# Performance work log

Hardware: AMD Instinct MI355X
Metric: run time of the kernel (lower is better)

Reference implementation:

```python
import jax, jax.numpy as jnp
import numpy as np

FIELD_DIMS = 100000
FACTORS = 16
BATCH = 1024


def setup_inputs() -> dict:
    key = jax.random.key(0)
    k1, k2 = jax.random.split(key)
    # multi-hot indicator rows (values in {0,1}); row>0 selects active embedding rows
    x0 = jax.random.randint(k1, (BATCH, FIELD_DIMS), 0, 2, dtype=jnp.int32)
    # embedding table (truncated_normal init in the original; plain normal scaled is fine for a numeric reference)
    W = jax.random.normal(k2, (FIELD_DIMS, FACTORS), dtype=jnp.float32) * 0.05
    return {"x0": x0, "W": W}


def reference(x0, W):
    # Original per-row math: let E = W[row > 0] (active embedding rows)
    #   out = 0.5 * ( sum_{i,j} e_i . e_j  -  sum_i ||e_i||^2 )
    # sum_{i,j} e_i . e_j == || sum_i e_i ||^2, so with multi-hot mask m:
    #   s  = m @ W                     -> [B, k]
    #   q  = m @ rowwise_sumsq(W)      -> [B]
    #   out = 0.5 * (||s||^2 - q)      -> [B]
    m = (x0 > 0).astype(W.dtype)                    # [B, F]
    s = m @ W                                        # [B, k]
    q = m @ jnp.sum(W * W, axis=-1)                  # [B]
    return 0.5 * (jnp.sum(s * s, axis=-1) - q)
```

## Files before the change

kernel.cpp:

```cpp
#include <hip/hip_runtime.h>

#define FIELDS  100000
#define FACTORS 16
#define BATCH   1024
#define BT      8
#define NCHUNK  8
#define FPC     (FIELDS / NCHUNK)
#define BLOCK   256
#define TF      256
#define NFULL   (FPC / TF)
#define TAILPG  ((FPC - NFULL * TF) / 4)
#define NBUF    3

typedef __attribute__((address_space(1))) const void gvoid;
typedef __attribute__((address_space(3))) void lvoid;

__global__ __launch_bounds__(BLOCK, 4) void fm_partial(
    const int* __restrict__ x0, const float* __restrict__ W,
    float* __restrict__ ws)
{
    __shared__ __align__(16) int xbuf[NBUF][BT][TF];
    __shared__ float red[4][BT][17];

    const int t     = threadIdx.x;
    const int bid   = blockIdx.x;
    const int rg    = bid >> 3;
    const int chunk = bid & (NCHUNK - 1);
    const int b0    = rg * BT;
    const int fbeg  = chunk * FPC;

    const int qr   = t & 3;
    const int pg   = t >> 2;
    const int lane = t & 63;
    const int wv   = t >> 6;

    float acc[BT][4], qac[BT];
#pragma unroll
    for (int r = 0; r < BT; ++r) {
        qac[r] = 0.f;
#pragma unroll
        for (int j = 0; j < 4; ++j) acc[r][j] = 0.f;
    }

    const char* x0b = (const char*)x0;
    const char* Wb  = (const char*)W;

    const int r0 = 2 * wv, r1 = r0 + 1;
    const unsigned sb0 = ((unsigned)(b0 + r0) * FIELDS + (unsigned)fbeg) * 4u
                       + (unsigned)lane * 16u;
    const unsigned sb1 = sb0 + FIELDS * 4u;
    char* const l0 = (char*)&xbuf[0][r0][0] + lane * 16;
    char* const l1 = (char*)&xbuf[0][r1][0] + lane * 16;

#define STAGE(buf, tile) do {                                               \
        __builtin_amdgcn_global_load_lds(                                   \
            (gvoid*)(x0b + (sb0 + (unsigned)(tile) * (TF * 4u))),           \
            (lvoid*)(l0 + (buf) * (BT * TF * 4)), 16, 0, 0);                \
        __builtin_amdgcn_global_load_lds(                                   \
            (gvoid*)(x0b + (sb1 + (unsigned)(tile) * (TF * 4u))),           \
            (lvoid*)(l1 + (buf) * (BT * TF * 4)), 16, 0, 0);                \
    } while (0)

#define FMTILE(BUFEXPR)                                                     \
    do {                                                                    \
        const float s0 = fmaf(w0.x, w0.x, fmaf(w0.y, w0.y, fmaf(w0.z, w0.z, w0.w * w0.w))); \
        const float s1 = fmaf(w1.x, w1.x, fmaf(w1.y, w1.y, fmaf(w1.z, w1.z, w1.w * w1.w))); \
        const float s2 = fmaf(w2.x, w2.x, fmaf(w2.y, w2.y, fmaf(w2.z, w2.z, w2.w * w2.w))); \
        const float s3 = fmaf(w3.x, w3.x, fmaf(w3.y, w3.y, fmaf(w3.z, w3.z, w3.w * w3.w))); \
        _Pragma("unroll")                                                   \
        for (int r = 0; r < BT; ++r) {                                      \
            const int4 xv = BUFEXPR;                                        \
            const float m0 = (float)xv.x, m1 = (float)xv.y;                 \
            const float m2 = (float)xv.z, m3 = (float)xv.w;                 \
            qac[r]    = fmaf(m0, s0,   fmaf(m1, s1,   fmaf(m2, s2,   fmaf(m3, s3,   qac[r])))); \
            acc[r][0] = fmaf(m0, w0.x, fmaf(m1, w1.x, fmaf(m2, w2.x, fmaf(m3, w3.x, acc[r][0])))); \
            acc[r][1] = fmaf(m0, w0.y, fmaf(m1, w1.y, fmaf(m2, w2.y, fmaf(m3, w3.y, acc[r][1])))); \
            acc[r][2] = fmaf(m0, w0.z, fmaf(m1, w1.z, fmaf(m2, w2.z, fmaf(m3, w3.z, acc[r][2])))); \
            acc[r][3] = fmaf(m0, w0.w, fmaf(m1, w1.w, fmaf(m2, w2.w, fmaf(m3, w3.w, acc[r][3])))); \
        }                                                                   \
    } while (0)

    STAGE(0, 0);
    STAGE(1, 1);

    const unsigned wq = (unsigned)qr * 16u;

    for (int tl = 0; tl < NFULL; ++tl) {
        const unsigned fB = (unsigned)(fbeg + tl * TF + pg * 4) * 64u + wq;
        const float4 w0 = *(const float4*)(Wb + fB);
        const float4 w1 = *(const float4*)(Wb + fB + 64u);
        const float4 w2 = *(const float4*)(Wb + fB + 128u);
        const float4 w3 = *(const float4*)(Wb + fB + 192u);

        if      (tl == 0)         asm volatile("s_waitcnt vmcnt(6)"  ::: "memory");
        else if (tl < NFULL - 1)  asm volatile("s_waitcnt vmcnt(10)" ::: "memory");
        else                      asm volatile("s_waitcnt vmcnt(8)"  ::: "memory");
        __builtin_amdgcn_s_barrier();
        __builtin_amdgcn_sched_barrier(0);

        if (tl + 2 < NFULL) STAGE((tl + 2) % NBUF, tl + 2);

        const int buf = tl % NBUF;
        FMTILE((*(const int4*)&xbuf[buf][r][pg * 4]));
        __builtin_amdgcn_sched_barrier(0);
    }

    {
        const bool valid = (pg < TAILPG);
        const int  pgc   = valid ? pg : (TAILPG - 1);
        const unsigned fb = (unsigned)(fbeg + NFULL * TF + pgc * 4);
        const unsigned wB = fb * 64u + wq;
        float4 w0 = *(const float4*)(Wb + wB);
        float4 w1 = *(const float4*)(Wb + wB + 64u);
        float4 w2 = *(const float4*)(Wb + wB + 128u);
        float4 w3 = *(const float4*)(Wb + wB + 192u);
        if (!valid) {
            w0.x=w0.y=w0.z=w0.w=0.f; w1.x=w1.y=w1.z=w1.w=0.f;
            w2.x=w2.y=w2.z=w2.w=0.f; w3.x=w3.y=w3.z=w3.w=0.f;
        }
        FMTILE((*(const int4*)(x0b + ((unsigned)(b0 + r) * FIELDS + fb) * 4u)));
    }

#pragma unroll
    for (int r = 0; r < BT; ++r) {
#pragma unroll
        for (int off = 4; off < 64; off <<= 1) {
            acc[r][0] += __shfl_xor(acc[r][0], off);
            acc[r][1] += __shfl_xor(acc[r][1], off);
            acc[r][2] += __shfl_xor(acc[r][2], off);
            acc[r][3] += __shfl_xor(acc[r][3], off);
        }
#pragma unroll
        for (int off = 1; off < 64; off <<= 1)
            qac[r] += __shfl_xor(qac[r], off);
    }

    if (lane < 4) {
#pragma unroll
        for (int r = 0; r < BT; ++r) {
#pragma unroll
            for (int j = 0; j < 4; ++j)
                red[wv][r][lane * 4 + j] = acc[r][j];
            if (lane == 0) red[wv][r][16] = qac[r];
        }
    }
    __syncthreads();
    if (t < BT * 17) {
        const int r = t / 17;
        const int j = t % 17;
        const float v = red[0][r][j] + red[1][r][j] + red[2][r][j] + red[3][r][j];
        ws[((size_t)(b0 + r) * NCHUNK + chunk) * 17 + j] = v;
    }
#undef STAGE
#undef FMTILE
}

__global__ __launch_bounds__(BLOCK) void fm_final(
    const float* __restrict__ ws, float* __restrict__ out)
{
    const int b = blockIdx.x * BLOCK + threadIdx.x;
    if (b < BATCH) {
        const float* pbase = ws + (size_t)b * NCHUNK * 17;
        float s[17];
#pragma unroll
        for (int j = 0; j < 17; ++j) s[j] = 0.f;
#pragma unroll
        for (int c = 0; c < NCHUNK; ++c)
#pragma unroll
            for (int j = 0; j < 17; ++j) s[j] += pbase[c * 17 + j];
        float ss = 0.f;
#pragma unroll
        for (int k = 0; k < FACTORS; ++k) ss += s[k] * s[k];
        out[b] = 0.5f * (ss - s[16]);
    }
}

extern "C" void kernel_launch(void* const* d_in, const int* in_sizes, int n_in,
                              void* d_out, int out_size, void* d_ws, size_t ws_size,
                              hipStream_t stream)
{
    const int*   x0 = (const int*)d_in[0];
    const float* W  = (const float*)d_in[1];
    float* out = (float*)d_out;
    float* ws  = (float*)d_ws;

    fm_partial<<<dim3((BATCH / BT) * NCHUNK), dim3(BLOCK), 0, stream>>>(x0, W, ws);
    fm_final<<<dim3((BATCH + BLOCK - 1) / BLOCK), dim3(BLOCK), 0, stream>>>(ws, out);
}
```

Measured before the change: 119.2 us.

## Double tile width to 512 fields with double-buffered LDS staging

Each pipeline step now covers 512 fields instead of 256. Each wave issues four async global-to-LDS loads per step, and each thread loads eight W float4s to cover both halves of the tile. The triple buffer that staged two tiles ahead becomes a double buffer that stages one tile ahead, with a single fixed vmcnt wait. The aim is to halve the barrier and loop overhead and give each wait more bytes in flight, at the cost of a shallower prefetch, more LDS and higher register pressure.

```diff
diff --git a/kernel.cpp b/kernel.cpp
--- a/kernel.cpp
+++ b/kernel.cpp
@@ -7,10 +7,10 @@
 #define NCHUNK  8
 #define FPC     (FIELDS / NCHUNK)
 #define BLOCK   256
-#define TF      256
-#define NFULL   (FPC / TF)
-#define TAILPG  ((FPC - NFULL * TF) / 4)
-#define NBUF    3
+#define TF      512
+#define NTF     (FPC / TF)
+#define TAILPG  ((FPC - NTF * TF) / 4)
+#define NBUF    2
 
 typedef __attribute__((address_space(1))) const void gvoid;
 typedef __attribute__((address_space(3))) void lvoid;
@@ -53,72 +53,80 @@
     char* const l1 = (char*)&xbuf[0][r1][0] + lane * 16;
 
 #define STAGE(buf, tile) do {                                               \
-        __builtin_amdgcn_global_load_lds(                                   \
-            (gvoid*)(x0b + (sb0 + (unsigned)(tile) * (TF * 4u))),           \
+        const unsigned _so = (unsigned)(tile) * (TF * 4u);                  \
+        __builtin_amdgcn_global_load_lds((gvoid*)(x0b + (sb0 + _so)),       \
             (lvoid*)(l0 + (buf) * (BT * TF * 4)), 16, 0, 0);                \
-        __builtin_amdgcn_global_load_lds(                                   \
-            (gvoid*)(x0b + (sb1 + (unsigned)(tile) * (TF * 4u))),           \
+        __builtin_amdgcn_global_load_lds((gvoid*)(x0b + (sb0 + _so + 1024u)),\
+            (lvoid*)(l0 + (buf) * (BT * TF * 4) + 1024), 16, 0, 0);         \
+        __builtin_amdgcn_global_load_lds((gvoid*)(x0b + (sb1 + _so)),       \
             (lvoid*)(l1 + (buf) * (BT * TF * 4)), 16, 0, 0);                \
+        __builtin_amdgcn_global_load_lds((gvoid*)(x0b + (sb1 + _so + 1024u)),\
+            (lvoid*)(l1 + (buf) * (BT * TF * 4) + 1024), 16, 0, 0);         \
     } while (0)
 
-#define FMTILE(BUFEXPR)                                                     \
+#define FMTILE(p0, p1, p2, p3, BUFEXPR)                                     \
     do {                                                                    \
-        const float s0 = fmaf(w0.x, w0.x, fmaf(w0.y, w0.y, fmaf(w0.z, w0.z, w0.w * w0.w))); \
-        const float s1 = fmaf(w1.x, w1.x, fmaf(w1.y, w1.y, fmaf(w1.z, w1.z, w1.w * w1.w))); \
-        const float s2 = fmaf(w2.x, w2.x, fmaf(w2.y, w2.y, fmaf(w2.z, w2.z, w2.w * w2.w))); \
-        const float s3 = fmaf(w3.x, w3.x, fmaf(w3.y, w3.y, fmaf(w3.z, w3.z, w3.w * w3.w))); \
+        const float s0 = fmaf(p0.x, p0.x, fmaf(p0.y, p0.y, fmaf(p0.z, p0.z, p0.w * p0.w))); \
+        const float s1 = fmaf(p1.x, p1.x, fmaf(p1.y, p1.y, fmaf(p1.z, p1.z, p1.w * p1.w))); \
+        const float s2 = fmaf(p2.x, p2.x, fmaf(p2.y, p2.y, fmaf(p2.z, p2.z, p2.w * p2.w))); \
+        const float s3 = fmaf(p3.x, p3.x, fmaf(p3.y, p3.y, fmaf(p3.z, p3.z, p3.w * p3.w))); \
         _Pragma("unroll")                                                   \
         for (int r = 0; r < BT; ++r) {                                      \
             const int4 xv = BUFEXPR;                                        \
             const float m0 = (float)xv.x, m1 = (float)xv.y;                 \
             const float m2 = (float)xv.z, m3 = (float)xv.w;                 \
             qac[r]    = fmaf(m0, s0,   fmaf(m1, s1,   fmaf(m2, s2,   fmaf(m3, s3,   qac[r])))); \
-            acc[r][0] = fmaf(m0, w0.x, fmaf(m1, w1.x, fmaf(m2, w2.x, fmaf(m3, w3.x, acc[r][0])))); \
-            acc[r][1] = fmaf(m0, w0.y, fmaf(m1, w1.y, fmaf(m2, w2.y, fmaf(m3, w3.y, acc[r][1])))); \
-            acc[r][2] = fmaf(m0, w0.z, fmaf(m1, w1.z, fmaf(m2, w2.z, fmaf(m3, w3.z, acc[r][2])))); \
-            acc[r][3] = fmaf(m0, w0.w, fmaf(m1, w1.w, fmaf(m2, w2.w, fmaf(m3, w3.w, acc[r][3])))); \
+            acc[r][0] = fmaf(m0, p0.x, fmaf(m1, p1.x, fmaf(m2, p2.x, fmaf(m3, p3.x, acc[r][0])))); \
+            acc[r][1] = fmaf(m0, p0.y, fmaf(m1, p1.y, fmaf(m2, p2.y, fmaf(m3, p3.y, acc[r][1])))); \
+            acc[r][2] = fmaf(m0, p0.z, fmaf(m1, p1.z, fmaf(m2, p2.z, fmaf(m3, p3.z, acc[r][2])))); \
+            acc[r][3] = fmaf(m0, p0.w, fmaf(m1, p1.w, fmaf(m2, p2.w, fmaf(m3, p3.w, acc[r][3])))); \
         }                                                                   \
     } while (0)
 
+    const unsigned wq = (unsigned)qr * 16u;
+    const unsigned wbase = (unsigned)(fbeg + pg * 4) * 64u + wq;
+
     STAGE(0, 0);
-    STAGE(1, 1);
 
-    const unsigned wq = (unsigned)qr * 16u;
+#pragma unroll 1
+    for (int tl = 0; tl < NTF; ++tl) {
+        const unsigned wB = wbase + (unsigned)tl * (TF * 64u);
+        const float4 wa0 = *(const float4*)(Wb + wB);
+        const float4 wa1 = *(const float4*)(Wb + wB + 64u);
+        const float4 wa2 = *(const float4*)(Wb + wB + 128u);
+        const float4 wa3 = *(const float4*)(Wb + wB + 192u);
+        const float4 wb0 = *(const float4*)(Wb + wB + 16384u);
+        const float4 wb1 = *(const float4*)(Wb + wB + 16384u + 64u);
+        const float4 wb2 = *(const float4*)(Wb + wB + 16384u + 128u);
+        const float4 wb3 = *(const float4*)(Wb + wB + 16384u + 192u);
 
-    for (int tl = 0; tl < NFULL; ++tl) {
-        const unsigned fB = (unsigned)(fbeg + tl * TF + pg * 4) * 64u + wq;
-        const float4 w0 = *(const float4*)(Wb + fB);
-        const float4 w1 = *(const float4*)(Wb + fB + 64u);
-        const float4 w2 = *(const float4*)(Wb + fB + 128u);
-        const float4 w3 = *(const float4*)(Wb + fB + 192u);
-
-        if      (tl == 0)         asm volatile("s_waitcnt vmcnt(6)"  ::: "memory");
-        else if (tl < NFULL - 1)  asm volatile("s_waitcnt vmcnt(10)" ::: "memory");
-        else                      asm volatile("s_waitcnt vmcnt(8)"  ::: "memory");
+        asm volatile("s_waitcnt vmcnt(8)" ::: "memory");
         __builtin_amdgcn_s_barrier();
         __builtin_amdgcn_sched_barrier(0);
 
-        if (tl + 2 < NFULL) STAGE((tl + 2) % NBUF, tl + 2);
+        if (tl + 1 < NTF) STAGE((tl + 1) & 1, tl + 1);
+        __builtin_amdgcn_sched_barrier(0);
 
-        const int buf = tl % NBUF;
-        FMTILE((*(const int4*)&xbuf[buf][r][pg * 4]));
-        __builtin_amdgcn_sched_barrier(0);
+        const int buf = tl & 1;
+        FMTILE(wa0, wa1, wa2, wa3, (*(const int4*)&xbuf[buf][r][pg * 4]));
+        FMTILE(wb0, wb1, wb2, wb3, (*(const int4*)&xbuf[buf][r][256 + pg * 4]));
     }
 
     {
         const bool valid = (pg < TAILPG);
         const int  pgc   = valid ? pg : (TAILPG - 1);
-        const unsigned fb = (unsigned)(fbeg + NFULL * TF + pgc * 4);
-        const unsigned wB = fb * 64u + wq;
-        float4 w0 = *(const float4*)(Wb + wB);
-        float4 w1 = *(const float4*)(Wb + wB + 64u);
-        float4 w2 = *(const float4*)(Wb + wB + 128u);
-        float4 w3 = *(const float4*)(Wb + wB + 192u);
+        const unsigned fb = (unsigned)(fbeg + NTF * TF + pgc * 4);
+        const unsigned wT = fb * 64u + wq;
+        float4 w0 = *(const float4*)(Wb + wT);
+        float4 w1 = *(const float4*)(Wb + wT + 64u);
+        float4 w2 = *(const float4*)(Wb + wT + 128u);
+        float4 w3 = *(const float4*)(Wb + wT + 192u);
         if (!valid) {
             w0.x=w0.y=w0.z=w0.w=0.f; w1.x=w1.y=w1.z=w1.w=0.f;
             w2.x=w2.y=w2.z=w2.w=0.f; w3.x=w3.y=w3.z=w3.w=0.f;
         }
-        FMTILE((*(const int4*)(x0b + ((unsigned)(b0 + r) * FIELDS + fb) * 4u)));
+        FMTILE(w0, w1, w2, w3,
+               (*(const int4*)(x0b + ((unsigned)(b0 + r) * FIELDS + fb) * 4u)));
     }
 
 #pragma unroll
```

Result: faster. 111.7 us (median of 2 runs) (-6.3%).
